# Kernel tuning notes

Hardware: AMD Instinct MI355X
Metric: run time of the kernel (lower is better)

The kernel has to match this reference:

```python
import jax, jax.numpy as jnp
import numpy as np
import math

H = 8        # num_heads
D = 1024     # per-head dim (d_q = d_k = d_v)
D_I = 1024   # image embed dim
D_L = 768    # sentence embed dim
EPS = 1e-5   # nn.LayerNorm default


def setup_inputs() -> dict:
    key = jax.random.key(0)
    ks = jax.random.split(key, 8)
    B, NQ, NK = 8, 196, 128
    img_embed = jax.random.normal(ks[0], (B, NQ, D_I), dtype=jnp.float32)
    sent_embed = jax.random.normal(ks[1], (B, NK, D_L), dtype=jnp.float32)
    atten_mask = jnp.ones((B, NK), dtype=jnp.int32)
    # weights stored [in, out] (equivalent to torch Linear weight.T), no bias
    Wq = jax.random.normal(ks[2], (D_I, H * D), dtype=jnp.float32) * (1.0 / math.sqrt(D_I))
    Wk = jax.random.normal(ks[3], (D_L, H * D), dtype=jnp.float32) * (1.0 / math.sqrt(D_L))
    Wv = jax.random.normal(ks[4], (D_L, H * D), dtype=jnp.float32) * (1.0 / math.sqrt(D_L))
    Wo = jax.random.normal(ks[5], (H * D, D_I), dtype=jnp.float32) * (1.0 / math.sqrt(H * D))
    gamma = jnp.ones((D_I,), dtype=jnp.float32)
    beta = jnp.zeros((D_I,), dtype=jnp.float32)
    return {"img_embed": img_embed, "sent_embed": sent_embed, "atten_mask": atten_mask,
            "Wq": Wq, "Wk": Wk, "Wv": Wv, "Wo": Wo, "gamma": gamma, "beta": beta}


def reference(img_embed, sent_embed, atten_mask, Wq, Wk, Wv, Wo, gamma, beta):
    B = img_embed.shape[0]
    # projections -> [B, N, H, D] -> [B, H, N, D]
    Q = (img_embed @ Wq).reshape(B, -1, H, D).transpose(0, 2, 1, 3)
    K = (sent_embed @ Wk).reshape(B, -1, H, D).transpose(0, 2, 1, 3)
    V = (sent_embed @ Wv).reshape(B, -1, H, D).transpose(0, 2, 1, 3)
    # scaled dot-product scores [B, H, NQ, NK]
    score = jnp.einsum('bhqd,bhkd->bhqk', Q, K) / math.sqrt(D)
    mask = (atten_mask != 0)[:, None, None, :]  # [B,1,1,NK]
    score = jnp.where(mask, score, -jnp.inf)
    attn = jax.nn.softmax(score, axis=-1)
    # PV -> [B, NQ, H, D] -> [B, NQ, H*D]
    ctx = jnp.einsum('bhqk,bhkd->bqhd', attn, V).reshape(B, -1, H * D)
    out = ctx @ Wo + img_embed  # residual
    # LayerNorm over last dim
    mu = jnp.mean(out, axis=-1, keepdims=True)
    var = jnp.var(out, axis=-1, keepdims=True)
    return (out - mu) * jax.lax.rsqrt(var + EPS) * gamma + beta
```

## Files before the change

### kernel.cpp

```cpp
#include <hip/hip_runtime.h>
#include <hip/hip_bf16.h>

#define BB 8
#define NQ 196
#define NKK 128
#define HH 8
#define DH 1024
#define DI 1024
#define DL 768
#define HD 8192
#define KSPLIT 8

typedef __attribute__((ext_vector_type(8))) short short8;
typedef __attribute__((ext_vector_type(4))) float f32x4;

__device__ inline unsigned short f2bf(float f) {
  unsigned int x = __float_as_uint(f);
  unsigned int r = (x + 0x7fffu + ((x >> 16) & 1u)) >> 16;
  return (unsigned short)r;
}

__device__ inline void gload16(const unsigned short* g, unsigned short* l) {
  __builtin_amdgcn_global_load_lds(
      (const __attribute__((address_space(1))) void*)g,
      (__attribute__((address_space(3))) void*)l, 16, 0, 0);
}

__global__ __launch_bounds__(256) void k_f32_to_bf16(
    const float* __restrict__ in, unsigned short* __restrict__ out, int n) {
  int i = (blockIdx.x * 256 + threadIdx.x) * 8;
  if (i >= n) return;
  float4 x = *reinterpret_cast<const float4*>(in + i);
  float4 y = *reinterpret_cast<const float4*>(in + i + 4);
  short8 v;
  v[0] = (short)f2bf(x.x); v[1] = (short)f2bf(x.y);
  v[2] = (short)f2bf(x.z); v[3] = (short)f2bf(x.w);
  v[4] = (short)f2bf(y.x); v[5] = (short)f2bf(y.y);
  v[6] = (short)f2bf(y.z); v[7] = (short)f2bf(y.w);
  *reinterpret_cast<short8*>(out + i) = v;
}

__global__ __launch_bounds__(256) void k_transpose_all(
    const float* __restrict__ Wq, const float* __restrict__ Wk,
    const float* __restrict__ Wv, const float* __restrict__ Wo,
    unsigned short* __restrict__ WqT, unsigned short* __restrict__ WkvT,
    unsigned short* __restrict__ WoT) {
  int b = blockIdx.x;
  const float* in; unsigned short* out; int R, C, bx;
  if (b < 8192)       { in = Wq; out = WqT;  R = DI; C = HD; bx = b; }
  else if (b < 14336) { in = Wk; out = WkvT; R = DL; C = HD; bx = b - 8192; }
  else if (b < 20480) { in = Wv; out = WkvT + (size_t)HD * DL; R = DL; C = HD; bx = b - 14336; }
  else                { in = Wo; out = WoT;  R = HD; C = DI; bx = b - 20480; }
  int nxc = C / 32;
  int c0 = (bx % nxc) * 32, r0 = (bx / nxc) * 32;
  __shared__ float tile[32][33];
  {
    int rr = threadIdx.x >> 3, c4 = (threadIdx.x & 7) << 2;
    float4 v = *reinterpret_cast<const float4*>(&in[(size_t)(r0 + rr) * C + c0 + c4]);
    tile[rr][c4] = v.x; tile[rr][c4 + 1] = v.y;
    tile[rr][c4 + 2] = v.z; tile[rr][c4 + 3] = v.w;
  }
  __syncthreads();
  {
    int cc = threadIdx.x >> 3, r4 = (threadIdx.x & 7) << 2;
    ushort4 w;
    w.x = f2bf(tile[r4][cc]);     w.y = f2bf(tile[r4 + 1][cc]);
    w.z = f2bf(tile[r4 + 2][cc]); w.w = f2bf(tile[r4 + 3][cc]);
    *reinterpret_cast<ushort4*>(&out[(size_t)(c0 + cc) * R + r0 + r4]) = w;
  }
}

__global__ __launch_bounds__(256) void k_transpose_v(
    const unsigned short* __restrict__ Vp, unsigned short* __restrict__ Vt, int ld_in) {
  __shared__ unsigned short tile[32][34];
  int z = blockIdx.z, b = z >> 3, h = z & 7;
  const unsigned short* in = Vp + (size_t)b * NKK * ld_in + (size_t)h * DH;
  unsigned short* out = Vt + (size_t)z * DH * NKK;
  int d0 = blockIdx.x * 32, k0 = blockIdx.y * 32;
  {
    int rr = threadIdx.x >> 3, c4 = (threadIdx.x & 7) << 2;
    ushort4 v = *reinterpret_cast<const ushort4*>(&in[(size_t)(k0 + rr) * ld_in + d0 + c4]);
    tile[rr][c4] = v.x; tile[rr][c4 + 1] = v.y;
    tile[rr][c4 + 2] = v.z; tile[rr][c4 + 3] = v.w;
  }
  __syncthreads();
  {
    int cc = threadIdx.x >> 3, r4 = (threadIdx.x & 7) << 2;
    ushort4 w;
    w.x = tile[r4][cc];     w.y = tile[r4 + 1][cc];
    w.z = tile[r4 + 2][cc]; w.w = tile[r4 + 3][cc];
    *reinterpret_cast<ushort4*>(&out[(size_t)(d0 + cc) * NKK + k0 + r4]) = w;
  }
}


__device__ __attribute__((always_inline)) inline void ph_pre() {
  __builtin_amdgcn_s_barrier();
  asm volatile("s_waitcnt lgkmcnt(0)" ::: "memory");
  __builtin_amdgcn_sched_barrier(0);
  __builtin_amdgcn_s_setprio(1);
}
__device__ __attribute__((always_inline)) inline void ph_post() {
  __builtin_amdgcn_s_setprio(0);
  __builtin_amdgcn_s_barrier();
}
__device__ __attribute__((always_inline)) inline void ph_post_vm4() {
  __builtin_amdgcn_s_setprio(0);
  asm volatile("s_waitcnt vmcnt(4)" ::: "memory");
  __builtin_amdgcn_s_barrier();
}
__device__ __attribute__((always_inline)) inline void ph_post_vm0() {
  __builtin_amdgcn_s_setprio(0);
  asm volatile("s_waitcnt vmcnt(0)" ::: "memory");
  __builtin_amdgcn_s_barrier();
}

#define LDA8(d, buf, s)                                                          \
  { _Pragma("unroll") for (int mi = 0; mi < 4; ++mi) {                           \
      const int row_ = wm * 128 + (s) * 64 + mi * 16 + fr;                       \
      d[mi][0] = *reinterpret_cast<const short8*>(&As[buf][row_ * 64 + swz0]);   \
      d[mi][1] = *reinterpret_cast<const short8*>(&As[buf][row_ * 64 + swz1]);   \
    } }
#define LDB8(d, buf, s)                                                          \
  { _Pragma("unroll") for (int ni = 0; ni < 2; ++ni) {                           \
      const int row_ = wn * 64 + (s) * 32 + ni * 16 + fr;                        \
      d[ni][0] = *reinterpret_cast<const short8*>(&Bs[buf][row_ * 64 + swz0]);   \
      d[ni][1] = *reinterpret_cast<const short8*>(&Bs[buf][row_ * 64 + swz1]);   \
    } }
#define MMQ(a, sa, b, sb)                                                        \
  { _Pragma("unroll") for (int kk = 0; kk < 2; ++kk) {                           \
      _Pragma("unroll") for (int mi = 0; mi < 4; ++mi) {                         \
        _Pragma("unroll") for (int ni = 0; ni < 2; ++ni)                         \
          acc[(sa) * 4 + mi][(sb) * 2 + ni] =                                    \
              __builtin_amdgcn_mfma_f32_16x16x32_bf16(                           \
                  a[mi][kk], b[ni][kk], acc[(sa) * 4 + mi][(sb) * 2 + ni], 0, 0, 0); \
      } } }
#define STA8(buf, h, kof)                                                        \
  { gload16(aS[h][0] + (kof), &As[buf][(h) * 8192 + wid * 512]);                 \
    gload16(aS[h][1] + (kof), &As[buf][(h) * 8192 + 4096 + wid * 512]); }
#define STB8(buf, h, kof)                                                        \
  { gload16(bS[h][0] + (kof), &Bs[buf][(h) * 8192 + wid * 512]);                 \
    gload16(bS[h][1] + (kof), &Bs[buf][(h) * 8192 + 4096 + wid * 512]); }

template<bool C_BF16>
__global__ __launch_bounds__(512, 2) void k_gemm8(
    const unsigned short* __restrict__ A, const unsigned short* __restrict__ B,
    void* __restrict__ Cptr,
    int M, int K, int lda, int ldb, int ldc,
    int nx, int ny, int ZBH,
    long aSB, long aSH, long bSB, long bSH, long cSB, long cSH,
    long aKC, long bKC, long cKC) {
  __shared__ unsigned short As[2][16384];
  __shared__ unsigned short Bs[2][16384];

  const int qq = gridDim.x >> 3;
  int g; { const int o = blockIdx.x; g = (o & 7) * qq + (o >> 3); }
  const int ybl = g % ny; int t1 = g / ny;
  const int xbl = t1 % nx; const int zz = t1 / nx;
  const int kc = zz / ZBH, bh = zz % ZBH;
  const int zb = bh >> 3, zh = bh & 7;

  const unsigned short* Ab = A + (size_t)zb * aSB + (size_t)zh * aSH + (size_t)kc * aKC;
  const unsigned short* Bb = B + (size_t)zb * bSB + (size_t)zh * bSH + (size_t)kc * bKC;

  const int tid = threadIdx.x, lane = tid & 63, wid = tid >> 6;
  const int wm = wid >> 2, wn = wid & 3;
  const int m_base = ybl * 256, n_base = xbl * 256;
  const int fr = lane & 15, qk = lane >> 4;
  const int swz0 = ((qk ^ (fr & 7)) << 3);
  const int swz1 = (((4 + qk) ^ (fr & 7)) << 3);

  const int srow = lane >> 3;
  const int sc8 = (((lane & 7) ^ srow) << 3);
  const unsigned short* aS[2][2];
  const unsigned short* bS[2][2];
#pragma unroll
  for (int h = 0; h < 2; ++h)
#pragma unroll
    for (int j = 0; j < 2; ++j) {
      int rm = m_base + h * 128 + j * 64 + wid * 8 + srow;
      rm = rm < M ? rm : M - 1;
      aS[h][j] = Ab + (size_t)rm * lda + sc8;
      bS[h][j] = Bb + (size_t)(n_base + h * 128 + j * 64 + wid * 8 + srow) * ldb + sc8;
    }

  short8 a0[4][2], a1[4][2], b0[2][2], b1[2][2];
  f32x4 acc[8][4] = {};

  const int NT = K >> 6;
  const int NIT = NT >> 1;

  STB8(0, 0, 0) STB8(0, 1, 0) STA8(0, 0, 0) STA8(0, 1, 0)
  STB8(1, 0, 64) STB8(1, 1, 64)
  asm volatile("s_waitcnt vmcnt(4)" ::: "memory");
  __builtin_amdgcn_s_barrier();

  for (int it = 0; it < NIT - 1; ++it) {
    const int t1k = (2 * it + 1) << 6;
    const int t2k = (2 * it + 2) << 6;
    const int t3k = (2 * it + 3) << 6;
    LDA8(a0, 0, 0) LDB8(b0, 0, 0) STA8(1, 0, t1k)
    ph_pre(); MMQ(a0, 0, b0, 0) ph_post();
    LDB8(b1, 0, 1) STA8(1, 1, t1k)
    ph_pre(); MMQ(a0, 0, b1, 1) ph_post();
    LDA8(a1, 0, 1) STB8(0, 0, t2k)
    ph_pre(); MMQ(a1, 1, b1, 1) ph_post();
    STB8(0, 1, t2k)
    ph_pre(); MMQ(a1, 1, b0, 0) ph_post_vm4();
    LDA8(a0, 1, 0) LDB8(b0, 1, 0) STA8(0, 0, t2k)
    ph_pre(); MMQ(a0, 0, b0, 0) ph_post();
    LDB8(b1, 1, 1) STA8(0, 1, t2k)
    ph_pre(); MMQ(a0, 0, b1, 1) ph_post();
    LDA8(a1, 1, 1) STB8(1, 0, t3k)
    ph_pre(); MMQ(a1, 1, b1, 1) ph_post();
    STB8(1, 1, t3k)
    ph_pre(); MMQ(a1, 1, b0, 0) ph_post_vm4();
  }

  {
    const int tlk = (NT - 1) << 6;
    LDA8(a0, 0, 0) LDB8(b0, 0, 0) STA8(1, 0, tlk)
    ph_pre(); MMQ(a0, 0, b0, 0) ph_post();
    LDB8(b1, 0, 1) STA8(1, 1, tlk)
    ph_pre(); MMQ(a0, 0, b1, 1) ph_post();
    LDA8(a1, 0, 1)
    ph_pre(); MMQ(a1, 1, b1, 1) ph_post();
    ph_pre(); MMQ(a1, 1, b0, 0) ph_post_vm0();
    LDA8(a0, 1, 0) LDB8(b0, 1, 0)
    ph_pre(); MMQ(a0, 0, b0, 0) ph_post();
    LDB8(b1, 1, 1)
    ph_pre(); MMQ(a0, 0, b1, 1) ph_post();
    LDA8(a1, 1, 1)
    ph_pre(); MMQ(a1, 1, b1, 1) ph_post();
    ph_pre(); MMQ(a1, 1, b0, 0)
    __builtin_amdgcn_s_setprio(0);
  }

  const size_t cOff = (size_t)zb * cSB + (size_t)zh * cSH + (size_t)kc * cKC;
  const int rq4 = qk * 4;
#pragma unroll
  for (int mi = 0; mi < 8; ++mi) {
#pragma unroll
    for (int ni = 0; ni < 4; ++ni) {
      int col = n_base + wn * 64 + ni * 16 + fr;
#pragma unroll
      for (int i = 0; i < 4; ++i) {
        int row = m_base + wm * 128 + mi * 16 + rq4 + i;
        if (row < M) {
          float val = acc[mi][ni][i];
          size_t off = cOff + (size_t)row * ldc + col;
          if constexpr (C_BF16) ((unsigned short*)Cptr)[off] = f2bf(val);
          else                  ((float*)Cptr)[off] = val;
        }
      }
    }
  }
}

template<bool C_BF16>
__global__ __launch_bounds__(256, 2) void k_gemm3(
    const unsigned short* __restrict__ A, const unsigned short* __restrict__ B,
    void* __restrict__ Cptr,
    int M, int K, int lda, int ldb, int ldc,
    int nx, int ny, int ZBH,
    long aSB, long aSH, long bSB, long bSH, long cSB, long cSH,
    long aKC, long bKC, long cKC) {
  __shared__ unsigned short As[8192];
  __shared__ unsigned short Bs[8192];

  const int nblk = gridDim.x;
  const int qq = nblk >> 3, rr = nblk & 7;
  int g;
  { const int o = blockIdx.x, xcd = o & 7, i = o >> 3;
    g = (xcd < rr ? xcd * (qq + 1) : rr * (qq + 1) + (xcd - rr) * qq) + i; }
  const int ybl = g % ny; int t1 = g / ny;
  const int xbl = t1 % nx; const int zz = t1 / nx;
  const int kc = zz / ZBH, bh = zz % ZBH;
  const int zb = bh >> 3, zh = bh & 7;

  const unsigned short* Ab = A + (size_t)zb * aSB + (size_t)zh * aSH + (size_t)kc * aKC;
  const unsigned short* Bb = B + (size_t)zb * bSB + (size_t)zh * bSH + (size_t)kc * bKC;

  const int tid = threadIdx.x, lane = tid & 63, wid = tid >> 6;
  const int wm = wid >> 1, wn = wid & 1;
  const int m_base = ybl * 128, n_base = xbl * 128;

  const int r0 = wid * 32 + (lane >> 3);
  const int sc8 = (((lane & 7) ^ (lane >> 3)) << 3);
  const unsigned short* aSrc[4];
  const unsigned short* bSrc[4];
#pragma unroll
  for (int p = 0; p < 4; ++p) {
    int rm = m_base + r0 + p * 8; rm = rm < M ? rm : M - 1;
    aSrc[p] = Ab + (size_t)rm * lda + sc8;
    bSrc[p] = Bb + (size_t)(n_base + r0 + p * 8) * ldb + sc8;
  }

  const int fr = lane & 15;
  const int qk = lane >> 4;
  f32x4 acc[4][4] = {};

  for (int k0 = 0; k0 < K; k0 += 64) {
#pragma unroll
    for (int p = 0; p < 4; ++p) gload16(aSrc[p] + k0, &As[wid * 2048 + p * 512]);
#pragma unroll
    for (int p = 0; p < 4; ++p) gload16(bSrc[p] + k0, &Bs[wid * 2048 + p * 512]);
    __syncthreads();
#pragma unroll
    for (int kk = 0; kk < 2; ++kk) {
      short8 af[4], bfr[4];
#pragma unroll
      for (int mi = 0; mi < 4; ++mi) {
        int row = wm * 64 + mi * 16 + fr;
        int swz = ((kk * 4 + qk) ^ (row & 7)) << 3;
        af[mi] = *reinterpret_cast<const short8*>(&As[row * 64 + swz]);
      }
#pragma unroll
      for (int ni = 0; ni < 4; ++ni) {
        int row = wn * 64 + ni * 16 + fr;
        int swz = ((kk * 4 + qk) ^ (row & 7)) << 3;
        bfr[ni] = *reinterpret_cast<const short8*>(&Bs[row * 64 + swz]);
      }
#pragma unroll
      for (int mi = 0; mi < 4; ++mi)
#pragma unroll
        for (int ni = 0; ni < 4; ++ni)
          acc[mi][ni] = __builtin_amdgcn_mfma_f32_16x16x32_bf16(af[mi], bfr[ni], acc[mi][ni], 0, 0, 0);
    }
    __syncthreads();
  }

  const size_t cOff = (size_t)zb * cSB + (size_t)zh * cSH + (size_t)kc * cKC;
  const int rq = qk * 4;
#pragma unroll
  for (int mi = 0; mi < 4; ++mi) {
#pragma unroll
    for (int ni = 0; ni < 4; ++ni) {
      int col = n_base + wn * 64 + ni * 16 + fr;
#pragma unroll
      for (int i = 0; i < 4; ++i) {
        int row = m_base + wm * 64 + mi * 16 + rq + i;
        if (row < M) {
          float val = acc[mi][ni][i];
          size_t off = cOff + (size_t)row * ldc + col;
          if constexpr (C_BF16) ((unsigned short*)Cptr)[off] = f2bf(val);
          else                  ((float*)Cptr)[off] = val;
        }
      }
    }
  }
}

#define S_PART ((size_t)64 * NQ * NKK)
__global__ __launch_bounds__(256) void k_softmax(
    const float* __restrict__ S, unsigned short* __restrict__ P, const int* __restrict__ mask) {
  int row = blockIdx.x * 4 + (threadIdx.x >> 6);
  if (row >= BB * HH * NQ) return;
  int lane = threadIdx.x & 63;
  int b = row / (HH * NQ);
  const float* s = S + (size_t)row * NKK;
  float s0 = (s[lane]      + s[lane + S_PART])      * 0.03125f;
  float s1 = (s[lane + 64] + s[lane + 64 + S_PART]) * 0.03125f;
  const int* mrow = mask + b * NKK;
  if (mrow[lane] == 0)      s0 = -1e30f;
  if (mrow[lane + 64] == 0) s1 = -1e30f;
  float mx = fmaxf(s0, s1);
#pragma unroll
  for (int d = 32; d; d >>= 1) mx = fmaxf(mx, __shfl_xor(mx, d));
  float e0 = __expf(s0 - mx), e1 = __expf(s1 - mx);
  float sum = e0 + e1;
#pragma unroll
  for (int d = 32; d; d >>= 1) sum += __shfl_xor(sum, d);
  float inv = 1.0f / sum;
  P[(size_t)row * NKK + lane]      = f2bf(e0 * inv);
  P[(size_t)row * NKK + lane + 64] = f2bf(e1 * inv);
}

__global__ __launch_bounds__(256) void k_layernorm_red(
    const float* __restrict__ Parts, const float* __restrict__ resid,
    const float* __restrict__ gamma, const float* __restrict__ beta,
    float* __restrict__ out, int M) {
  int row = blockIdx.x;
  int tid = threadIdx.x;
  const size_t stride = (size_t)M * DI;
  const float* p = Parts + (size_t)row * DI;
  const float* r = resid + (size_t)row * DI;
  float v[4], sum = 0.f, sq = 0.f;
#pragma unroll
  for (int i = 0; i < 4; ++i) {
    int c = tid + i * 256;
    float acc = r[c];
#pragma unroll
    for (int k = 0; k < KSPLIT; ++k) acc += p[k * stride + c];
    v[i] = acc; sum += acc; sq += acc * acc;
  }
#pragma unroll
  for (int d = 32; d; d >>= 1) { sum += __shfl_xor(sum, d); sq += __shfl_xor(sq, d); }
  __shared__ float ssum[4], ssq[4];
  int w = tid >> 6;
  if ((tid & 63) == 0) { ssum[w] = sum; ssq[w] = sq; }
  __syncthreads();
  sum = ssum[0] + ssum[1] + ssum[2] + ssum[3];
  sq  = ssq[0]  + ssq[1]  + ssq[2]  + ssq[3];
  float mean = sum * (1.0f / DI);
  float var  = sq * (1.0f / DI) - mean * mean;
  float rstd = rsqrtf(var + 1e-5f);
  float* o = out + (size_t)row * DI;
#pragma unroll
  for (int i = 0; i < 4; ++i) {
    int c = tid + i * 256;
    o[c] = (v[i] - mean) * rstd * gamma[c] + beta[c];
  }
}

extern "C" void kernel_launch(void* const* d_in, const int* in_sizes, int n_in,
                              void* d_out, int out_size, void* d_ws, size_t ws_size,
                              hipStream_t stream) {
  const float* img   = (const float*)d_in[0];
  const float* sent  = (const float*)d_in[1];
  const int*   mask  = (const int*)d_in[2];
  const float* Wq    = (const float*)d_in[3];
  const float* Wk    = (const float*)d_in[4];
  const float* Wv    = (const float*)d_in[5];
  const float* Wo    = (const float*)d_in[6];
  const float* gamma = (const float*)d_in[7];
  const float* beta  = (const float*)d_in[8];
  float* out = (float*)d_out;

  char* ws = (char*)d_ws;
  unsigned short* WoT   = (unsigned short*)(ws);
  unsigned short* WkvT  = (unsigned short*)(ws + 16777216);
  unsigned short* Vt    = (unsigned short*)(ws + 16777216);
  float*          Oac   = (float*)         (ws + 16777216);
  float*          S2    = (float*)         (ws + 33554432);
  unsigned short* P     = (unsigned short*)(ws + 46399488);
  unsigned short* Qb    = (unsigned short*)(ws + 49610752);
  unsigned short* KVb   = (unsigned short*)(ws + 75300864);
  unsigned short* ctx   = (unsigned short*)(ws + 75300864);
  unsigned short* WqT   = (unsigned short*)(ws + 75300864);
  unsigned short* imgB  = (unsigned short*)(ws + 92078080);
  unsigned short* sentB = (unsigned short*)(ws + 108855296);

  dim3 tb(256);
  dim3 tb8(512);

  k_f32_to_bf16<<<dim3((BB * NQ * DI) / 2048), tb, 0, stream>>>(img, imgB, BB * NQ * DI);
  k_f32_to_bf16<<<dim3((BB * NKK * DL) / 2048), tb, 0, stream>>>(sent, sentB, BB * NKK * DL);
  k_transpose_all<<<dim3(28672), tb, 0, stream>>>(Wq, Wk, Wv, Wo, WqT, WkvT, WoT);

  k_gemm8<true><<<dim3(7 * 32), tb8, 0, stream>>>(
      imgB, WqT, Qb, BB * NQ, DI, DI, DI, HD,
      32, 7, 1, 0, 0, 0, 0, 0, 0, 0, 0, 0);

  k_gemm8<true><<<dim3(4 * 64), tb8, 0, stream>>>(
      sentB, WkvT, KVb, BB * NKK, DL, DL, DL, 2 * HD,
      64, 4, 1, 0, 0, 0, 0, 0, 0, 0, 0, 0);

  k_transpose_v<<<dim3(DH / 32, NKK / 32, BB * HH), tb, 0, stream>>>(KVb + HD, Vt, 2 * HD);

  k_gemm3<false><<<dim3(2 * 1 * 128), tb, 0, stream>>>(
      Qb, KVb, S2, NQ, DH / 2, HD, 2 * HD, NKK,
      1, 2, 64,
      (long)NQ * HD, (long)DH, (long)NKK * 2 * HD, (long)DH,
      (long)HH * NQ * NKK, (long)NQ * NKK,
      (long)(DH / 2), (long)(DH / 2), (long)64 * NQ * NKK);

  k_softmax<<<dim3(BB * HH * NQ / 4), tb, 0, stream>>>(S2, P, mask);

  k_gemm3<true><<<dim3(2 * 8 * 64), tb, 0, stream>>>(
      P, Vt, ctx, NQ, NKK, NKK, NKK, HD,
      8, 2, 64,
      (long)HH * NQ * NKK, (long)NQ * NKK, (long)HH * DH * NKK, (long)DH * NKK,
      (long)NQ * HD, (long)DH, 0, 0, 0);

  k_gemm8<false><<<dim3(7 * 4 * KSPLIT), tb8, 0, stream>>>(
      ctx, WoT, Oac, BB * NQ, HD / KSPLIT, HD, HD, DI,
      4, 7, 1, 0, 0, 0, 0, 0, 0,
      (long)(HD / KSPLIT), (long)(HD / KSPLIT), (long)(BB * NQ) * DI);

  k_layernorm_red<<<dim3(BB * NQ), tb, 0, stream>>>(Oac, img, gamma, beta, out, BB * NQ);
}
```

Measured before the change: 197.0 us.

## Merge prep kernels, batch Q and KV GEMMs, deepen GEMM prefetch

Combines the two f32-to-bf16 conversions and the weight transposes into a single prep kernel that uses 64x64 transpose tiles and 16-byte stores. Launches the Q and KV projection GEMMs as one grid, with blocks split between two configurations, to cut launch overhead and fill the device better. It also changes the GEMM global-to-LDS prefetch schedule so one more A half-tile is in flight (vmcnt 4 to 6). The aim is fewer launches, wider memory accesses and more load/compute overlap, at the cost of a larger LDS tile in the prep kernel and more outstanding loads in the GEMM.

```diff
diff --git a/kernel.cpp b/kernel.cpp
--- a/kernel.cpp
+++ b/kernel.cpp
@@ -26,47 +26,51 @@
       (__attribute__((address_space(3))) void*)l, 16, 0, 0);
 }
 
-__global__ __launch_bounds__(256) void k_f32_to_bf16(
-    const float* __restrict__ in, unsigned short* __restrict__ out, int n) {
-  int i = (blockIdx.x * 256 + threadIdx.x) * 8;
-  if (i >= n) return;
-  float4 x = *reinterpret_cast<const float4*>(in + i);
-  float4 y = *reinterpret_cast<const float4*>(in + i + 4);
-  short8 v;
-  v[0] = (short)f2bf(x.x); v[1] = (short)f2bf(x.y);
-  v[2] = (short)f2bf(x.z); v[3] = (short)f2bf(x.w);
-  v[4] = (short)f2bf(y.x); v[5] = (short)f2bf(y.y);
-  v[6] = (short)f2bf(y.z); v[7] = (short)f2bf(y.w);
-  *reinterpret_cast<short8*>(out + i) = v;
-}
-
-__global__ __launch_bounds__(256) void k_transpose_all(
+__global__ __launch_bounds__(256) void k_prep(
     const float* __restrict__ Wq, const float* __restrict__ Wk,
     const float* __restrict__ Wv, const float* __restrict__ Wo,
+    const float* __restrict__ img, const float* __restrict__ sent,
     unsigned short* __restrict__ WqT, unsigned short* __restrict__ WkvT,
-    unsigned short* __restrict__ WoT) {
-  int b = blockIdx.x;
+    unsigned short* __restrict__ WoT,
+    unsigned short* __restrict__ imgB, unsigned short* __restrict__ sentB) {
+  int b = blockIdx.x, t = threadIdx.x;
+  if (b >= 7168) {
+    const float* in; unsigned short* out; int i;
+    if (b < 7952) { in = img;  out = imgB;  i = ((b - 7168) * 256 + t) * 8; }
+    else          { in = sent; out = sentB; i = ((b - 7952) * 256 + t) * 8; }
+    float4 x = *reinterpret_cast<const float4*>(in + i);
+    float4 y = *reinterpret_cast<const float4*>(in + i + 4);
+    short8 v;
+    v[0] = (short)f2bf(x.x); v[1] = (short)f2bf(x.y);
+    v[2] = (short)f2bf(x.z); v[3] = (short)f2bf(x.w);
+    v[4] = (short)f2bf(y.x); v[5] = (short)f2bf(y.y);
+    v[6] = (short)f2bf(y.z); v[7] = (short)f2bf(y.w);
+    *reinterpret_cast<short8*>(out + i) = v;
+    return;
+  }
   const float* in; unsigned short* out; int R, C, bx;
-  if (b < 8192)       { in = Wq; out = WqT;  R = DI; C = HD; bx = b; }
-  else if (b < 14336) { in = Wk; out = WkvT; R = DL; C = HD; bx = b - 8192; }
-  else if (b < 20480) { in = Wv; out = WkvT + (size_t)HD * DL; R = DL; C = HD; bx = b - 14336; }
-  else                { in = Wo; out = WoT;  R = HD; C = DI; bx = b - 20480; }
-  int nxc = C / 32;
-  int c0 = (bx % nxc) * 32, r0 = (bx / nxc) * 32;
-  __shared__ float tile[32][33];
-  {
-    int rr = threadIdx.x >> 3, c4 = (threadIdx.x & 7) << 2;
-    float4 v = *reinterpret_cast<const float4*>(&in[(size_t)(r0 + rr) * C + c0 + c4]);
-    tile[rr][c4] = v.x; tile[rr][c4 + 1] = v.y;
-    tile[rr][c4 + 2] = v.z; tile[rr][c4 + 3] = v.w;
+  if (b < 2048)      { in = Wq; out = WqT;  R = DI; C = HD; bx = b; }
+  else if (b < 3584) { in = Wk; out = WkvT; R = DL; C = HD; bx = b - 2048; }
+  else if (b < 5120) { in = Wv; out = WkvT + (size_t)HD * DL; R = DL; C = HD; bx = b - 3584; }
+  else               { in = Wo; out = WoT;  R = HD; C = DI; bx = b - 5120; }
+  int nxc = C >> 6;
+  int c0 = (bx % nxc) << 6, r0 = (bx / nxc) << 6;
+  __shared__ float tile[64][65];
+#pragma unroll
+  for (int p = 0; p < 4; ++p) {
+    int row = p * 16 + (t >> 4), c4 = (t & 15) << 2;
+    float4 v = *reinterpret_cast<const float4*>(&in[(size_t)(r0 + row) * C + c0 + c4]);
+    tile[row][c4] = v.x; tile[row][c4 + 1] = v.y;
+    tile[row][c4 + 2] = v.z; tile[row][c4 + 3] = v.w;
   }
   __syncthreads();
-  {
-    int cc = threadIdx.x >> 3, r4 = (threadIdx.x & 7) << 2;
-    ushort4 w;
-    w.x = f2bf(tile[r4][cc]);     w.y = f2bf(tile[r4 + 1][cc]);
-    w.z = f2bf(tile[r4 + 2][cc]); w.w = f2bf(tile[r4 + 3][cc]);
-    *reinterpret_cast<ushort4*>(&out[(size_t)(c0 + cc) * R + r0 + r4]) = w;
+#pragma unroll
+  for (int p = 0; p < 2; ++p) {
+    int cc = p * 32 + (t >> 3), r8 = (t & 7) << 3;
+    short8 w;
+#pragma unroll
+    for (int j = 0; j < 8; ++j) w[j] = (short)f2bf(tile[r8 + j][cc]);
+    *reinterpret_cast<short8*>(&out[(size_t)(c0 + cc) * R + r0 + r8]) = w;
   }
 }
 
@@ -104,9 +108,9 @@
   __builtin_amdgcn_s_setprio(0);
   __builtin_amdgcn_s_barrier();
 }
-__device__ __attribute__((always_inline)) inline void ph_post_vm4() {
+__device__ __attribute__((always_inline)) inline void ph_post_vm6() {
   __builtin_amdgcn_s_setprio(0);
-  asm volatile("s_waitcnt vmcnt(4)" ::: "memory");
+  asm volatile("s_waitcnt vmcnt(6)" ::: "memory");
   __builtin_amdgcn_s_barrier();
 }
 __device__ __attribute__((always_inline)) inline void ph_post_vm0() {
@@ -142,26 +146,29 @@
   { gload16(bS[h][0] + (kof), &Bs[buf][(h) * 8192 + wid * 512]);                 \
     gload16(bS[h][1] + (kof), &Bs[buf][(h) * 8192 + 4096 + wid * 512]); }
 
+struct GCfg {
+  const unsigned short* A; const unsigned short* B; void* C;
+  int M, K, lda, ldb, ldc, nx, ny;
+  long aKC, bKC, cKC;
+};
+
 template<bool C_BF16>
-__global__ __launch_bounds__(512, 2) void k_gemm8(
-    const unsigned short* __restrict__ A, const unsigned short* __restrict__ B,
-    void* __restrict__ Cptr,
-    int M, int K, int lda, int ldb, int ldc,
-    int nx, int ny, int ZBH,
-    long aSB, long aSH, long bSB, long bSH, long cSB, long cSH,
-    long aKC, long bKC, long cKC) {
+__global__ __launch_bounds__(512, 2) void k_gemm8(GCfg c0, GCfg c1, int split) {
   __shared__ unsigned short As[2][16384];
   __shared__ unsigned short Bs[2][16384];
 
-  const int qq = gridDim.x >> 3;
-  int g; { const int o = blockIdx.x; g = (o & 7) * qq + (o >> 3); }
-  const int ybl = g % ny; int t1 = g / ny;
-  const int xbl = t1 % nx; const int zz = t1 / nx;
-  const int kc = zz / ZBH, bh = zz % ZBH;
-  const int zb = bh >> 3, zh = bh & 7;
-
-  const unsigned short* Ab = A + (size_t)zb * aSB + (size_t)zh * aSH + (size_t)kc * aKC;
-  const unsigned short* Bb = B + (size_t)zb * bSB + (size_t)zh * bSH + (size_t)kc * bKC;
+  const int seg = (int)blockIdx.x >= split;
+  const GCfg cfg = seg ? c1 : c0;
+  const int o = (int)blockIdx.x - (seg ? split : 0);
+  const int nseg = seg ? ((int)gridDim.x - split) : split;
+  const int qq = nseg >> 3;
+  const int g = (o & 7) * qq + (o >> 3);
+  const int ybl = g % cfg.ny; int t1 = g / cfg.ny;
+  const int xbl = t1 % cfg.nx; const int kc = t1 / cfg.nx;
+
+  const int M = cfg.M, lda = cfg.lda, ldb = cfg.ldb;
+  const unsigned short* Ab = cfg.A + (size_t)kc * cfg.aKC;
+  const unsigned short* Bb = cfg.B + (size_t)kc * cfg.bKC;
 
   const int tid = threadIdx.x, lane = tid & 63, wid = tid >> 6;
   const int wm = wid >> 2, wn = wid & 3;
@@ -187,41 +194,41 @@
   short8 a0[4][2], a1[4][2], b0[2][2], b1[2][2];
   f32x4 acc[8][4] = {};
 
-  const int NT = K >> 6;
+  const int NT = cfg.K >> 6;
   const int NIT = NT >> 1;
 
   STB8(0, 0, 0) STB8(0, 1, 0) STA8(0, 0, 0) STA8(0, 1, 0)
-  STB8(1, 0, 64) STB8(1, 1, 64)
-  asm volatile("s_waitcnt vmcnt(4)" ::: "memory");
+  STB8(1, 0, 64) STB8(1, 1, 64) STA8(1, 0, 64)
+  asm volatile("s_waitcnt vmcnt(6)" ::: "memory");
   __builtin_amdgcn_s_barrier();
 
   for (int it = 0; it < NIT - 1; ++it) {
     const int t1k = (2 * it + 1) << 6;
     const int t2k = (2 * it + 2) << 6;
     const int t3k = (2 * it + 3) << 6;
-    LDA8(a0, 0, 0) LDB8(b0, 0, 0) STA8(1, 0, t1k)
+    LDA8(a0, 0, 0) LDB8(b0, 0, 0) STA8(1, 1, t1k)
     ph_pre(); MMQ(a0, 0, b0, 0) ph_post();
-    LDB8(b1, 0, 1) STA8(1, 1, t1k)
+    LDB8(b1, 0, 1)
     ph_pre(); MMQ(a0, 0, b1, 1) ph_post();
     LDA8(a1, 0, 1) STB8(0, 0, t2k)
     ph_pre(); MMQ(a1, 1, b1, 1) ph_post();
-    STB8(0, 1, t2k)
-    ph_pre(); MMQ(a1, 1, b0, 0) ph_post_vm4();
-    LDA8(a0, 1, 0) LDB8(b0, 1, 0) STA8(0, 0, t2k)
+    STB8(0, 1, t2k) STA8(0, 0, t2k)
+    ph_pre(); MMQ(a1, 1, b0, 0) ph_post_vm6();
+    LDA8(a0, 1, 0) LDB8(b0, 1, 0) STA8(0, 1, t2k)
     ph_pre(); MMQ(a0, 0, b0, 0) ph_post();
-    LDB8(b1, 1, 1) STA8(0, 1, t2k)
+    LDB8(b1, 1, 1)
     ph_pre(); MMQ(a0, 0, b1, 1) ph_post();
     LDA8(a1, 1, 1) STB8(1, 0, t3k)
     ph_pre(); MMQ(a1, 1, b1, 1) ph_post();
-    STB8(1, 1, t3k)
-    ph_pre(); MMQ(a1, 1, b0, 0) ph_post_vm4();
+    STB8(1, 1, t3k) STA8(1, 0, t3k)
+    ph_pre(); MMQ(a1, 1, b0, 0) ph_post_vm6();
   }
 
   {
     const int tlk = (NT - 1) << 6;
-    LDA8(a0, 0, 0) LDB8(b0, 0, 0) STA8(1, 0, tlk)
+    LDA8(a0, 0, 0) LDB8(b0, 0, 0) STA8(1, 1, tlk)
     ph_pre(); MMQ(a0, 0, b0, 0) ph_post();
-    LDB8(b1, 0, 1) STA8(1, 1, tlk)
+    LDB8(b1, 0, 1)
     ph_pre(); MMQ(a0, 0, b1, 1) ph_post();
     LDA8(a1, 0, 1)
     ph_pre(); MMQ(a1, 1, b1, 1) ph_post();
@@ -236,7 +243,8 @@
     __builtin_amdgcn_s_setprio(0);
   }
 
-  const size_t cOff = (size_t)zb * cSB + (size_t)zh * cSH + (size_t)kc * cKC;
+  const size_t cOff = (size_t)kc * cfg.cKC;
+  const int ldc = cfg.ldc;
   const int rq4 = qk * 4;
 #pragma unroll
   for (int mi = 0; mi < 8; ++mi) {
@@ -249,8 +257,8 @@
         if (row < M) {
           float val = acc[mi][ni][i];
           size_t off = cOff + (size_t)row * ldc + col;
-          if constexpr (C_BF16) ((unsigned short*)Cptr)[off] = f2bf(val);
-          else                  ((float*)Cptr)[off] = val;
+          if constexpr (C_BF16) ((unsigned short*)cfg.C)[off] = f2bf(val);
+          else                  ((float*)cfg.C)[off] = val;
         }
       }
     }
@@ -444,17 +452,12 @@
   dim3 tb(256);
   dim3 tb8(512);
 
-  k_f32_to_bf16<<<dim3((BB * NQ * DI) / 2048), tb, 0, stream>>>(img, imgB, BB * NQ * DI);
-  k_f32_to_bf16<<<dim3((BB * NKK * DL) / 2048), tb, 0, stream>>>(sent, sentB, BB * NKK * DL);
-  k_transpose_all<<<dim3(28672), tb, 0, stream>>>(Wq, Wk, Wv, Wo, WqT, WkvT, WoT);
-
-  k_gemm8<true><<<dim3(7 * 32), tb8, 0, stream>>>(
-      imgB, WqT, Qb, BB * NQ, DI, DI, DI, HD,
-      32, 7, 1, 0, 0, 0, 0, 0, 0, 0, 0, 0);
-
-  k_gemm8<true><<<dim3(4 * 64), tb8, 0, stream>>>(
-      sentB, WkvT, KVb, BB * NKK, DL, DL, DL, 2 * HD,
-      64, 4, 1, 0, 0, 0, 0, 0, 0, 0, 0, 0);
+  k_prep<<<dim3(8336), tb, 0, stream>>>(Wq, Wk, Wv, Wo, img, sent,
+                                        WqT, WkvT, WoT, imgB, sentB);
+
+  GCfg cfgQ  = { imgB,  WqT,  Qb,  BB * NQ,  DI, DI, DI, HD,      32, 7, 0, 0, 0 };
+  GCfg cfgKV = { sentB, WkvT, KVb, BB * NKK, DL, DL, DL, 2 * HD,  64, 4, 0, 0, 0 };
+  k_gemm8<true><<<dim3(224 + 256), tb8, 0, stream>>>(cfgQ, cfgKV, 224);
 
   k_transpose_v<<<dim3(DH / 32, NKK / 32, BB * HH), tb, 0, stream>>>(KVb + HD, Vt, 2 * HD);
 
@@ -473,10 +476,9 @@
       (long)HH * NQ * NKK, (long)NQ * NKK, (long)HH * DH * NKK, (long)DH * NKK,
       (long)NQ * HD, (long)DH, 0, 0, 0);
 
-  k_gemm8<false><<<dim3(7 * 4 * KSPLIT), tb8, 0, stream>>>(
-      ctx, WoT, Oac, BB * NQ, HD / KSPLIT, HD, HD, DI,
-      4, 7, 1, 0, 0, 0, 0, 0, 0,
-      (long)(HD / KSPLIT), (long)(HD / KSPLIT), (long)(BB * NQ) * DI);
+  GCfg cfgO = { ctx, WoT, Oac, BB * NQ, HD / KSPLIT, HD, HD, DI, 4, 7,
+                (long)(HD / KSPLIT), (long)(HD / KSPLIT), (long)(BB * NQ) * DI };
+  k_gemm8<false><<<dim3(224), tb8, 0, stream>>>(cfgO, cfgO, 224);
 
   k_layernorm_red<<<dim3(BB * NQ), tb, 0, stream>>>(Oac, img, gamma, beta, out, BB * NQ);
 }
```

After: 190.8 us. 1.03x faster.
